# Kernel optimization log

Measured on AMD Instinct MI355X. Metric: run time of the kernel, lower is better.

Reference implementation:

```python
import jax, jax.numpy as jnp
import numpy as np

B, L, HIDDEN = 64, 200, 256
HEADS = 8
MAX_WIDTH = 5
EPS = 1e-5  # F.layer_norm default eps


def _ln(x):
    # F.layer_norm with no learned affine
    m = jnp.mean(x, axis=-1, keepdims=True)
    v = jnp.mean((x - m) ** 2, axis=-1, keepdims=True)
    return (x - m) * jax.lax.rsqrt(v + EPS)


def _area_pool(x, max_width, mode):
    # x: [B, H, L, D] -> pooled spans of widths 1..max_width (valid windows),
    # concatenated along the memory axis: M = sum_w (L - w + 1)
    Lx = x.shape[2]
    outs = []
    for w in range(1, max_width + 1):
        # [w, B, H, L-w+1, D] stack of shifted slices (w <= 5, tiny loop)
        win = jnp.stack([x[:, :, i:Lx - w + 1 + i, :] for i in range(w)], axis=0)
        if mode == 'max':
            outs.append(win.max(axis=0))
        elif mode == 'mean':
            outs.append(win.mean(axis=0))
        else:  # 'sum'
            outs.append(win.sum(axis=0))
    return jnp.concatenate(outs, axis=2)


def _mha_area(q_in, k_in, v_in, Wq, bq, Wk, bk, Wv, bv, Wo, bo):
    # per-head size equals hidden_size (key_query_size_hidden = hidden_size)
    Bq, Lq, _ = q_in.shape
    Dh = Wq.shape[1] // HEADS

    def split(x):
        return x.reshape(x.shape[0], x.shape[1], HEADS, Dh).transpose(0, 2, 1, 3)

    q = split(q_in @ Wq + bq)  # [B, H, Lq, Dh]
    k = split(k_in @ Wk + bk)
    v = split(v_in @ Wv + bv)
    k_area = _area_pool(k, MAX_WIDTH, 'max')   # aggr='max' key pooling
    v_area = _area_pool(v, MAX_WIDTH, 'sum')   # values pooled by sum (t2t default)
    scale = jnp.asarray(1.0 / np.sqrt(Dh), q.dtype)
    logits = jnp.einsum('bhqd,bhmd->bhqm', q, k_area) * scale
    attn = jax.nn.softmax(logits, axis=-1)  # dropout inactive at eval
    out = jnp.einsum('bhqm,bhmd->bhqd', attn, v_area)
    out = out.transpose(0, 2, 1, 3).reshape(Bq, Lq, HEADS * Dh)
    return out @ Wo + bo


def setup_inputs() -> dict:
    key = jax.random.key(0)
    ks = jax.random.split(key, 16)
    stdv = 1.0 / np.sqrt(HIDDEN)
    u = lambda k, shp: jax.random.uniform(k, shp, jnp.float32, -stdv, stdv)
    HD = HEADS * HIDDEN  # 2048
    return {
        'A': jax.random.normal(ks[0], (B, L, L), jnp.float32),
        'hidden': jax.random.normal(ks[1], (B, L, HIDDEN), jnp.float32),
        'Wq': u(ks[2], (HIDDEN, HD)), 'bq': u(ks[3], (HD,)),
        'Wk': u(ks[4], (HIDDEN, HD)), 'bk': u(ks[5], (HD,)),
        'Wv': u(ks[6], (HIDDEN, HD)), 'bv': u(ks[7], (HD,)),
        'Wo': u(ks[8], (HD, HIDDEN)), 'bo': u(ks[9], (HIDDEN,)),
        'W1': u(ks[10], (HIDDEN, 4 * HIDDEN)), 'b1': u(ks[11], (4 * HIDDEN,)),
        'W2': u(ks[12], (4 * HIDDEN, HIDDEN)), 'b2': u(ks[13], (HIDDEN,)),
    }


def reference(A, hidden, Wq, bq, Wk, bk, Wv, bv, Wo, bo, W1, b1, W2, b2):
    # step = 1 -> single ATTNCell; A is unused by ATTNCell (matches source)
    attn1 = _mha_area(hidden, hidden, hidden, Wq, bq, Wk, bk, Wv, bv, Wo, bo)
    attn1 = _ln(attn1 + hidden)
    attn2 = _mha_area(attn1, hidden, hidden, Wq, bq, Wk, bk, Wv, bv, Wo, bo)
    attn2 = _ln(attn1 + attn2)  # F.dropout inactive (eval)
    x = jax.nn.relu(attn2 @ W1 + b1) @ W2 + b2
    return _ln(attn2 + x)
```

## Files before the change

kernel.cpp:

```cpp
#include <hip/hip_runtime.h>
#include <hip/hip_bf16.h>
#include <cstdint>
#include <cstddef>

#define BATCH 64
#define LSEQ 200
#define HID 256
#define NH 8
#define DH 256
#define HD (NH*DH)
#define MROWS (BATCH*LSEQ)
#define EPS 1e-5f
#define CSCALE 0.09014195f

typedef unsigned short ushort_t;
typedef __attribute__((ext_vector_type(8))) short bf16x8;
typedef __attribute__((ext_vector_type(8))) unsigned short u16x8;
typedef __attribute__((ext_vector_type(4))) float f32x4;

__device__ __forceinline__ float b2f(ushort_t u) {
    union { unsigned int i; float f; } c; c.i = ((unsigned int)u) << 16; return c.f;
}
__device__ __forceinline__ ushort_t f2b(float f) {
    __hip_bfloat16 h = __float2bfloat16(f);
    union { __hip_bfloat16 h; ushort_t u; } c; c.h = h; return c.u;
}
__device__ __forceinline__ float to_f32(float x) { return x; }
__device__ __forceinline__ float to_f32(ushort_t x) { return b2f(x); }
__device__ __forceinline__ void store_val(float* p, float v) { *p = v; }
__device__ __forceinline__ void store_val(ushort_t* p, float v) { *p = f2b(v); }

__device__ __forceinline__ u16x8 bmax8(u16x8 a, u16x8 b) {
    union U { u16x8 v; __hip_bfloat162 h[4]; };
    U ua, ub, r; ua.v = a; ub.v = b;
    #pragma unroll
    for (int i = 0; i < 4; ++i) r.h[i] = __hmax2(ua.h[i], ub.h[i]);
    return r.v;
}
__device__ __forceinline__ u16x8 badd8(u16x8 a, u16x8 b) {
    union U { u16x8 v; __hip_bfloat162 h[4]; };
    U ua, ub, r; ua.v = a; ub.v = b;
    #pragma unroll
    for (int i = 0; i < 4; ++i) r.h[i] = __hadd2(ua.h[i], ub.h[i]);
    return r.v;
}

__device__ __forceinline__ void gll16(const void* g, void* l) {
    __builtin_amdgcn_global_load_lds(
        (const __attribute__((address_space(1))) unsigned int*)g,
        (__attribute__((address_space(3))) unsigned int*)l, 16, 0, 0);
}

template<bool RELU, int OMODE, bool SCALEC>
__global__ __launch_bounds__(256) void gemm_bt(
    const ushort_t* __restrict__ A, const ushort_t* __restrict__ Bt,
    const float* __restrict__ bias, ushort_t* __restrict__ C,
    int M, int N, int K)
{
    __shared__ ushort_t As[128 * 32];
    __shared__ ushort_t Bs[128 * 32];
    const int t = threadIdx.x;
    const int m0 = blockIdx.y * 128, n0 = blockIdx.x * 128;
    const int wave = t >> 6, lane = t & 63;
    const int l15 = lane & 15, lq = lane >> 4;
    const int wr = wave >> 1, wc = wave & 1;

    f32x4 acc[4][4];
    #pragma unroll
    for (int i = 0; i < 4; ++i)
        #pragma unroll
        for (int j = 0; j < 4; ++j) acc[i][j] = (f32x4){0.f, 0.f, 0.f, 0.f};

    for (int k0 = 0; k0 < K; k0 += 32) {
        __syncthreads();
        #pragma unroll
        for (int i = 0; i < 2; ++i) {
            int li = i * 256 + t;
            int ml = li >> 2, cp = li & 3;
            int cg = cp ^ ((ml ^ (ml >> 2)) & 3);
            gll16(A + (size_t)(m0 + ml) * K + k0 + cg * 8, &As[li * 8]);
        }
        #pragma unroll
        for (int i = 0; i < 2; ++i) {
            int li = i * 256 + t;
            int nl = li >> 2, cp = li & 3;
            int cg = cp ^ ((nl ^ (nl >> 2)) & 3);
            gll16(Bt + (size_t)(n0 + nl) * K + k0 + cg * 8, &Bs[li * 8]);
        }
        __syncthreads();
        bf16x8 af[4], bfr[4];
        #pragma unroll
        for (int i = 0; i < 4; ++i) {
            int r = wr * 64 + i * 16 + l15;
            int pc = lq ^ ((r ^ (r >> 2)) & 3);
            af[i] = *(const bf16x8*)&As[r * 32 + pc * 8];
        }
// ... 2 lines not shown
            int r = wc * 64 + j * 16 + l15;
            int pc = lq ^ ((r ^ (r >> 2)) & 3);
            bfr[j] = *(const bf16x8*)&Bs[r * 32 + pc * 8];
        }
        #pragma unroll
        for (int i = 0; i < 4; ++i)
            #pragma unroll
            for (int j = 0; j < 4; ++j)
                acc[i][j] = __builtin_amdgcn_mfma_f32_16x16x32_bf16(af[i], bfr[j], acc[i][j], 0, 0, 0);
    }
    if (OMODE == 2) {
        #pragma unroll
        for (int i = 0; i < 4; ++i) {
            int mbase = m0 + wr * 64 + i * 16 + 4 * lq;
            int bb = (int)(((unsigned)mbase * 5243u) >> 20);
            int ll = mbase - bb * 200;
            #pragma unroll
            for (int j = 0; j < 4; ++j) {
                int n = n0 + wc * 64 + j * 16 + l15;
                float bsv = bias[n];
                ushort4 o4;
                o4.x = f2b(acc[i][j][0] + bsv); o4.y = f2b(acc[i][j][1] + bsv);
                o4.z = f2b(acc[i][j][2] + bsv); o4.w = f2b(acc[i][j][3] + bsv);
                size_t addr = ((size_t)(bb * NH + (n >> 8)) * 256 + (n & 255)) * LSEQ + ll;
                *(ushort4*)&C[addr] = o4;
            }
        }
    } else {
        #pragma unroll
        for (int i = 0; i < 4; ++i) {
            #pragma unroll
            for (int e = 0; e < 4; ++e) {
                int m = m0 + wr * 64 + i * 16 + 4 * lq + e;
                #pragma unroll
                for (int j = 0; j < 4; ++j) {
                    int n = n0 + wc * 64 + j * 16 + l15;
                    float v = acc[i][j][e] + bias[n];
                    if (RELU) v = fmaxf(v, 0.f);
                    if (SCALEC) v *= CSCALE;
                    if (OMODE == 1) {
                        int bb = (int)(((unsigned)m * 5243u) >> 20);
                        int ll = m - bb * 200;
                        size_t addr = ((((size_t)(bb * NH + (n >> 8))) * LSEQ + ll) << 8) + (n & 255);
                        C[addr] = f2b(v);
                    } else {
                        C[(size_t)m * N + n] = f2b(v);
                    }
                }
            }
        }
    }
}

__global__ __launch_bounds__(512, 2) void attn_mfma16(
    const ushort_t* __restrict__ Q, const ushort_t* __restrict__ Khm,
    const ushort_t* __restrict__ Vt, ushort_t* __restrict__ O)
{
    const int id = blockIdx.x;
    const int xcd = id & 7, slot_ = id >> 3;
    const int qt = slot_ & 1;
    const int bh = ((slot_ >> 1) << 3) + xcd;
    const int b = bh >> 3, h = bh & 7;
    const int q0 = qt * 128;
    const int t = threadIdx.x;
    const int wave = t >> 6, lane = t & 63;
    const int l15 = lane & 15, lq = lane >> 4;

    __shared__ ushort_t Ks[64 * 256];
    __shared__ ushort_t Vs[256 * 64];

    const ushort_t* kbh = Khm + (size_t)bh * LSEQ * DH;
    const ushort_t* vtb = Vt + (size_t)bh * DH * LSEQ;
    const ushort_t* qbh = Q + ((size_t)b * LSEQ) * HD + h * DH;
    const int qrow = q0 + wave * 16 + l15;

    bf16x8 qf[8];
    if (qrow < LSEQ) {
        const ushort_t* qp = qbh + (size_t)qrow * HD + 8 * lq;
        #pragma unroll
        for (int g = 0; g < 8; ++g) qf[g] = *(const bf16x8*)(qp + 32 * g);
    } else {
        bf16x8 zf = {0,0,0,0,0,0,0,0};
        #pragma unroll
        for (int g = 0; g < 8; ++g) qf[g] = zf;
    }

    f32x4 oacc[16];
    #pragma unroll
    for (int i = 0; i < 16; ++i) oacc[i] = (f32x4){0.f, 0.f, 0.f, 0.f};
    float l_part = 0.f;
    float carry[4];
    #pragma unroll
    for (int e = 0; e < 4; ++e) carry[e] = 0.f;

    const int dc = t & 31, mb = t >> 5;
    const int vd = t >> 1, vh = t & 1;

    auto shift1 = [&](float T[4][4]) {
        float up0 = __shfl(T[0][3], (lane - 16) & 63);
        float up1 = __shfl(T[1][3], (lane - 16) & 63);
        float up2 = __shfl(T[2][3], (lane - 16) & 63);
        float up3 = __shfl(T[3][3], (lane - 16) & 63);
        #pragma unroll
        for (int ms = 0; ms < 4; ++ms) {
            T[ms][3] = T[ms][2]; T[ms][2] = T[ms][1]; T[ms][1] = T[ms][0];
        }
        T[3][0] = (lq > 0) ? up3 : up2;
        T[2][0] = (lq > 0) ? up2 : up1;
        T[1][0] = (lq > 0) ? up1 : up0;
        T[0][0] = (lq > 0) ? up0 : 0.f;
    };

    auto pv32 = [&](const float P[4][4]) {
        unsigned int w[8];
        #pragma unroll
        for (int ms = 0; ms < 4; ++ms) {
            asm("v_cvt_pk_bf16_f32 %0, %1, %2" : "=v"(w[2*ms])   : "v"(P[ms][0]), "v"(P[ms][1]));
            asm("v_cvt_pk_bf16_f32 %0, %1, %2" : "=v"(w[2*ms+1]) : "v"(P[ms][2]), "v"(P[ms][3]));
        }
        union FR { unsigned int u[4]; bf16x8 v; };
        FR f0, f1;
        f0.u[0] = w[0]; f0.u[1] = w[1]; f0.u[2] = w[2]; f0.u[3] = w[3];
        f1.u[0] = w[4]; f1.u[1] = w[5]; f1.u[2] = w[6]; f1.u[3] = w[7];
        const bf16x8 pf0 = f0.v, pf1 = f1.v;
        __builtin_amdgcn_s_setprio(1);
        #pragma unroll
        for (int dt = 0; dt < 16; ++dt) {
            const int d = dt * 16 + l15;
            const int p0 = lq ^ (d & 7);
            const int p1 = (lq + 4) ^ (d & 7);
            oacc[dt] = __builtin_amdgcn_mfma_f32_16x16x32_bf16(
                           pf0, *(const bf16x8*)&Vs[d * 64 + p0 * 8], oacc[dt], 0, 0, 0);
            oacc[dt] = __builtin_amdgcn_mfma_f32_16x16x32_bf16(
                           pf1, *(const bf16x8*)&Vs[d * 64 + p1 * 8], oacc[dt], 0, 0, 0);
        }
        __builtin_amdgcn_s_setprio(0);
    };

    for (int ti = 0; ti < 3; ++ti) {
        const int st0 = ti * 64;
        float Pagg[4][4];
        {
            float pin0 = __shfl(carry[0], (lane + 48) & 63);
            float pin1 = __shfl(carry[1], (lane + 48) & 63);
            float pin2 = __shfl(carry[2], (lane + 48) & 63);
            float pin3 = __shfl(carry[3], (lane + 48) & 63);
            #pragma unroll
            for (int ms = 0; ms < 4; ++ms)
                #pragma unroll
                for (int e = 0; e < 4; ++e) Pagg[ms][e] = 0.f;
            if (lq == 0) {
                Pagg[0][0] = pin0; Pagg[0][1] = pin1; Pagg[0][2] = pin2; Pagg[0][3] = pin3;
            }
            #pragma unroll
            for (int e = 0; e < 4; ++e) carry[e] = 0.f;
        }
        #pragma unroll
        for (int cls = 0; cls < 5; ++cls) {
            u16x8 kf[4];
            #pragma unroll
            for (int k4 = 0; k4 < 4; ++k4)
                kf[k4] = *(const u16x8*)(kbh + (size_t)(st0 + mb + 16 * k4 + cls) * DH + dc * 8);
            u16x8 vc[4];
            if (cls == 0) {
                const ushort_t* vrow = vtb + (size_t)vd * LSEQ + st0 + vh * 32;
                #pragma unroll
                for (int c2 = 0; c2 < 4; ++c2) vc[c2] = *(const u16x8*)(vrow + c2 * 8);
            }
            __syncthreads();

            #pragma unroll
            for (int k4 = 0; k4 < 4; ++k4) {
                int m = mb + 16 * k4;
                ushort_t* kp = &Ks[m * 256 + ((dc ^ (m & 15)) * 8)];
                *(u16x8*)kp = (cls == 0) ? kf[k4] : bmax8(*(const u16x8*)kp, kf[k4]);
            }
            if (cls == 0) {
                #pragma unroll
                for (int cl = 0; cl < 4; ++cl) {
                    const int cg = vh * 4 + cl;
                    const int kc = (cg >> 2) * 4 + (cg & 1) * 2;
                    const int par4 = ((cg >> 1) & 1) * 4;
                    union VH { u16x8 v; ushort4 hh[2]; } nv;
                    nv.v = vc[cl];
                    *(ushort4*)&Vs[vd * 64 + ((kc ^ (vd & 7)) * 8) + par4] = nv.hh[0];
                    *(ushort4*)&Vs[vd * 64 + (((kc + 1) ^ (vd & 7)) * 8) + par4] = nv.hh[1];
                }
            }
            __syncthreads();

            f32x4 sacc[4];
            __builtin_amdgcn_s_setprio(1);
            #pragma unroll
            for (int ms = 0; ms < 4; ++ms) {
                f32x4 s = (f32x4){0.f, 0.f, 0.f, 0.f};
                const int row = ms * 16 + l15;
                #pragma unroll
                for (int g = 0; g < 8; ++g) {
                    const int phys = (lq + 4 * g) ^ l15;
                    s = __builtin_amdgcn_mfma_f32_16x16x32_bf16(
                            *(const bf16x8*)&Ks[row * 256 + phys * 8], qf[g], s, 0, 0, 0);
                }
                sacc[ms] = s;
            }
            __builtin_amdgcn_s_setprio(0);

            float Pc[4][4];
            #pragma unroll
            for (int ms = 0; ms < 4; ++ms)
                #pragma unroll
                for (int e = 0; e < 4; ++e) {
                    float pe = __builtin_exp2f(sacc[ms][e]);
                    l_part += pe;
                    Pc[ms][e] = pe;
                    Pagg[ms][e] += pe;
                }
            if (cls >= 1) {
                float T[4][4];
                #pragma unroll
                for (int ms = 0; ms < 4; ++ms)
                    #pragma unroll
                    for (int e = 0; e < 4; ++e) T[ms][e] = Pc[ms][e];
                #pragma unroll
                for (int u = 1; u <= 4; ++u) {
                    if (u <= cls) {
                        shift1(T);
                        #pragma unroll
                        for (int ms = 0; ms < 4; ++ms)
                            #pragma unroll
                            for (int e = 0; e < 4; ++e) Pagg[ms][e] += T[ms][e];
                    }
                }
            }
            #pragma unroll
            for (int i = 0; i < 4; ++i)
                #pragma unroll
                for (int e = 0; e < 4; ++e)
                    if (cls >= 4 + i - e) carry[i] += Pc[3][e];

            if (cls == 4) pv32(Pagg);
        }
    }

    {
        __syncthreads();
        if (mb < 8) {
            u16x8 krun = *(const u16x8*)(kbh + (size_t)(192 + mb) * DH + dc * 8);
            const u16x8 kz = {0,0,0,0,0,0,0,0};
            #pragma unroll
            for (int k8 = 0; k8 < 8; ++k8) {
                const bool v = (k8 <= 4) && (mb <= 7 - k8);
                if (k8 > 0 && v)
                    krun = bmax8(krun, *(const u16x8*)(kbh + (size_t)(192 + mb + k8) * DH + dc * 8));
                int slot = k8 * 8 + mb;
                *(u16x8*)&Ks[slot * 256 + ((dc ^ (slot & 15)) * 8)] = v ? krun : kz;
            }
        }
        {
            u16x8 v0 = *(const u16x8*)(vtb + (size_t)vd * LSEQ + 192);
            float f[8];
            #pragma unroll
            for (int e = 0; e < 8; ++e) f[e] = b2f(v0[e]);
            #pragma unroll
            for (int cl = 0; cl < 4; ++cl) {
                const int c = vh * 4 + cl;
                union VH { u16x8 v; ushort4 hh[2]; } ov;
                #pragma unroll
                for (int j = 0; j < 8; ++j) ov.v[j] = 0;
                if (c <= 4) {
                    #pragma unroll
                    for (int j = 0; j < 8; ++j) {
                        if (j <= 7 - c) {
                            float acc = 0.f;
                            #pragma unroll
                            for (int u = 0; u <= 4; ++u)
                                if (u <= c) acc += f[j + u];
                            ov.v[j] = f2b(acc);
                        }
                    }
                } else if (c == 5) {
                    #pragma unroll
                    for (int j = 0; j < 4; ++j) ov.v[j] = v0[j];
                }
                const int kc = (c >> 2) * 4 + (c & 1) * 2;
                const int par4 = ((c >> 1) & 1) * 4;
                *(ushort4*)&Vs[vd * 64 + ((kc ^ (vd & 7)) * 8) + par4] = ov.hh[0];
                *(ushort4*)&Vs[vd * 64 + (((kc + 1) ^ (vd & 7)) * 8) + par4] = ov.hh[1];
            }
        }
        __syncthreads();

        f32x4 sacc[4];
        __builtin_amdgcn_s_setprio(1);
        #pragma unroll
        for (int ms = 0; ms < 4; ++ms) {
            f32x4 s = (f32x4){0.f, 0.f, 0.f, 0.f};
            const int row = ms * 16 + l15;
            #pragma unroll
            for (int g = 0; g < 8; ++g) {
                const int phys = (lq + 4 * g) ^ l15;
                s = __builtin_amdgcn_mfma_f32_16x16x32_bf16(
                        *(const bf16x8*)&Ks[row * 256 + phys * 8], qf[g], s, 0, 0, 0);
            }
            sacc[ms] = s;
        }
        __builtin_amdgcn_s_setprio(0);

        float pullc[4];
        #pragma unroll
        for (int e = 0; e < 4; ++e) pullc[e] = __shfl(carry[e], (lane + 16) & 63);
        float Pt[4][4];
        #pragma unroll
        for (int ms = 0; ms < 4; ++ms)
            #pragma unroll
            for (int e = 0; e < 4; ++e) {
                const int slot = ms * 16 + 4 * lq + e;
                const bool inval = ((slot & 7) > 7 - (slot >> 3)) || ((slot >> 3) > 4);
                float pe = __builtin_exp2f(inval ? -1e30f : sacc[ms][e]);
                l_part += pe;
                float pfrag = pe;
                if (ms == 2 && lq == 2) pfrag = pullc[e];
                Pt[ms][e] = pfrag;
            }
        pv32(Pt);
    }

    l_part += __shfl_xor(l_part, 16);
    l_part += __shfl_xor(l_part, 32);
    const float inv = 1.f / l_part;

    ushort_t* ob = O + ((size_t)b * LSEQ) * HD + h * DH;
    #pragma unroll
    for (int e = 0; e < 4; ++e) {
        const int q = q0 + wave * 16 + 4 * lq + e;
        const float linv = __shfl(inv, 4 * lq + e);
        if (q < LSEQ) {
            #pragma unroll
            for (int dt = 0; dt < 16; ++dt)
                ob[(size_t)q * HD + dt * 16 + l15] = f2b(oacc[dt][e] * linv);
        }
    }
}

template<typename TR, typename TO>
__global__ __launch_bounds__(256) void residual_ln(
    const ushort_t* __restrict__ X, const TR* __restrict__ R, TO* __restrict__ Out)
{
    const int row = blockIdx.x;
    const int t = threadIdx.x;
    const size_t base = (size_t)row * HID;
    float v = b2f(X[base + t]) + to_f32(R[base + t]);
    float s = v, q = v * v;
    #pragma unroll
    for (int o = 32; o > 0; o >>= 1) {
        s += __shfl_xor(s, o, 64);
        q += __shfl_xor(q, o, 64);
    }
    __shared__ float ss[4], sq[4];
    const int wave = t >> 6, lane = t & 63;
    if (lane == 0) { ss[wave] = s; sq[wave] = q; }
    __syncthreads();
    s = ss[0] + ss[1] + ss[2] + ss[3];
    q = sq[0] + sq[1] + sq[2] + sq[3];
    float mean = s * (1.f / HID);
    float var  = q * (1.f / HID) - mean * mean;
    store_val(&Out[base + t], (v - mean) * rsqrtf(var + EPS));
}

__global__ __launch_bounds__(256) void cvt_f32_bf16(const float* __restrict__ in,
                                                    ushort_t* __restrict__ out) {
    const int i = (blockIdx.x * 256 + threadIdx.x) * 4;
    float4 v = *(const float4*)(in + i);
    ushort4 o;
    o.x = f2b(v.x); o.y = f2b(v.y); o.z = f2b(v.z); o.w = f2b(v.w);
    *(ushort4*)(out + i) = o;
}

__global__ __launch_bounds__(256) void wtrans(const float* __restrict__ W,
                                              ushort_t* __restrict__ Wt, int K, int N) {
// ... 11 lines not shown
}

extern "C" void kernel_launch(void* const* d_in, const int* in_sizes, int n_in,
                              void* d_out, int out_size, void* d_ws, size_t ws_size,
                              hipStream_t stream) {
    const float* hidden = (const float*)d_in[1];
    const float* Wq = (const float*)d_in[2];  const float* bq = (const float*)d_in[3];
    const float* Wk = (const float*)d_in[4];  const float* bk = (const float*)d_in[5];
    const float* Wv = (const float*)d_in[6];  const float* bv = (const float*)d_in[7];
    const float* Wo = (const float*)d_in[8];  const float* bo = (const float*)d_in[9];
    const float* W1 = (const float*)d_in[10]; const float* b1 = (const float*)d_in[11];
    const float* W2 = (const float*)d_in[12]; const float* b2 = (const float*)d_in[13];
    float* out = (float*)d_out;

    constexpr size_t SZ_BF   = (size_t)MROWS * HD * 2;
    constexpr size_t SZ_HBF  = (size_t)MROWS * HID * 2;
    constexpr size_t SZ_WQKV = (size_t)HID * HD * 2;
    constexpr size_t SZ_W12  = (size_t)HID * 4 * HID * 2;
    char* ws = (char*)d_ws;
    size_t off = 0;
    ushort_t* kb   = (ushort_t*)(ws + off); off += SZ_BF;
    ushort_t* vt   = (ushort_t*)(ws + off); off += SZ_BF;
    ushort_t* qo   = (ushort_t*)(ws + off); off += SZ_BF;
    ushort_t* hb   = (ushort_t*)(ws + off); off += SZ_HBF;
    ushort_t* at1  = (ushort_t*)(ws + off); off += SZ_HBF;
    ushort_t* at2  = (ushort_t*)(ws + off); off += SZ_HBF;
    ushort_t* proj = (ushort_t*)(ws + off); off += SZ_HBF;
    ushort_t* WtQ  = (ushort_t*)(ws + off); off += SZ_WQKV;
    ushort_t* WtK  = (ushort_t*)(ws + off); off += SZ_WQKV;
    ushort_t* WtV  = (ushort_t*)(ws + off); off += SZ_WQKV;
    ushort_t* WtO  = (ushort_t*)(ws + off); off += SZ_WQKV;
    ushort_t* Wt1  = (ushort_t*)(ws + off); off += SZ_W12;
    ushort_t* Wt2  = (ushort_t*)(ws + off); off += SZ_W12;
    if (ws_size < off) return;
    ushort_t* ffn1 = qo;

    dim3 blk(256);
    cvt_f32_bf16<<<MROWS * HID / 1024, blk, 0, stream>>>(hidden, hb);
    wtrans<<<dim3(HD / 32, HID / 32), blk, 0, stream>>>(Wq, WtQ, HID, HD);
    wtrans<<<dim3(HD / 32, HID / 32), blk, 0, stream>>>(Wk, WtK, HID, HD);
    wtrans<<<dim3(HD / 32, HID / 32), blk, 0, stream>>>(Wv, WtV, HID, HD);
    wtrans<<<dim3(HID / 32, HD / 32), blk, 0, stream>>>(Wo, WtO, HD, HID);
    wtrans<<<dim3(4 * HID / 32, HID / 32), blk, 0, stream>>>(W1, Wt1, HID, 4 * HID);
    wtrans<<<dim3(HID / 32, 4 * HID / 32), blk, 0, stream>>>(W2, Wt2, 4 * HID, HID);

    const dim3 gProj(HD / 128, MROWS / 128);
    const dim3 gOut(HID / 128, MROWS / 128);
    const dim3 gF1(4 * HID / 128, MROWS / 128);

    gemm_bt<false, 1, false><<<gProj, blk, 0, stream>>>(hb, WtK, bk, kb, MROWS, HD, HID);
    gemm_bt<false, 2, false><<<gProj, blk, 0, stream>>>(hb, WtV, bv, vt, MROWS, HD, HID);

    gemm_bt<false, 0, true><<<gProj, blk, 0, stream>>>(hb, WtQ, bq, qo, MROWS, HD, HID);
    attn_mfma16<<<2 * BATCH * NH, 512, 0, stream>>>(qo, kb, vt, qo);
    gemm_bt<false, 0, false><<<gOut, blk, 0, stream>>>(qo, WtO, bo, proj, MROWS, HID, HD);
    residual_ln<float, ushort_t><<<MROWS, blk, 0, stream>>>(proj, hidden, at1);

    gemm_bt<false, 0, true><<<gProj, blk, 0, stream>>>(at1, WtQ, bq, qo, MROWS, HD, HID);
    attn_mfma16<<<2 * BATCH * NH, 512, 0, stream>>>(qo, kb, vt, qo);
    gemm_bt<false, 0, false><<<gOut, blk, 0, stream>>>(qo, WtO, bo, proj, MROWS, HID, HD);
    residual_ln<ushort_t, ushort_t><<<MROWS, blk, 0, stream>>>(proj, at1, at2);

    gemm_bt<true, 0, false><<<gF1, blk, 0, stream>>>(at2, Wt1, b1, ffn1, MROWS, 4 * HID, HID);
    gemm_bt<false, 0, false><<<gOut, blk, 0, stream>>>(ffn1, Wt2, b2, proj, MROWS, HID, 4 * HID);
    residual_ln<ushort_t, float><<<MROWS, blk, 0, stream>>>(proj, at2, out);
}
```

Baseline: 902.3 us.

## Double-buffer K/V shared tiles in area attention to overlap loads with MFMA

Result: slower. 1.153 ms (+27.8%).

```diff
diff --git a/kernel.cpp b/kernel.cpp
--- a/kernel.cpp
+++ b/kernel.cpp
@@ -150,7 +150,7 @@
     }
 }
 
-__global__ __launch_bounds__(512, 2) void attn_mfma16(
+__global__ __launch_bounds__(512, 2) void attn_mfma17(
     const ushort_t* __restrict__ Q, const ushort_t* __restrict__ Khm,
     const ushort_t* __restrict__ Vt, ushort_t* __restrict__ O)
 {
@@ -164,8 +164,8 @@
     const int wave = t >> 6, lane = t & 63;
     const int l15 = lane & 15, lq = lane >> 4;
 
-    __shared__ ushort_t Ks[64 * 256];
-    __shared__ ushort_t Vs[256 * 64];
+    __shared__ ushort_t Ks[2 * 64 * 256];
+    __shared__ ushort_t Vs[2 * 256 * 64];
 
     const ushort_t* kbh = Khm + (size_t)bh * LSEQ * DH;
     const ushort_t* vtb = Vt + (size_t)bh * DH * LSEQ;
@@ -186,13 +186,47 @@
     f32x4 oacc[16];
     #pragma unroll
     for (int i = 0; i < 16; ++i) oacc[i] = (f32x4){0.f, 0.f, 0.f, 0.f};
-    float l_part = 0.f;
+    float l4[4];
+    #pragma unroll
+    for (int e = 0; e < 4; ++e) l4[e] = 0.f;
     float carry[4];
     #pragma unroll
     for (int e = 0; e < 4; ++e) carry[e] = 0.f;
 
     const int dc = t & 31, mb = t >> 5;
     const int vd = t >> 1, vh = t & 1;
+
+    u16x8 kr[4];
+
+    auto loadK = [&](u16x8* kf, int row0) {
+        #pragma unroll
+        for (int k4 = 0; k4 < 4; ++k4)
+            kf[k4] = *(const u16x8*)(kbh + (size_t)(row0 + mb + 16 * k4) * DH + dc * 8);
+    };
+    auto storeK = [&](int bo, const u16x8* kf) {
+        #pragma unroll
+        for (int k4 = 0; k4 < 4; ++k4) {
+            int m = mb + 16 * k4;
+            *(u16x8*)&Ks[bo + m * 256 + ((dc ^ (m & 15)) * 8)] = kf[k4];
+        }
+    };
+    auto loadV = [&](u16x8* vc, int s0) {
+        const ushort_t* vrow = vtb + (size_t)vd * LSEQ + s0 + vh * 32;
+        #pragma unroll
+        for (int c2 = 0; c2 < 4; ++c2) vc[c2] = *(const u16x8*)(vrow + c2 * 8);
+    };
+    auto storeV = [&](int bo, const u16x8* vc) {
+        #pragma unroll
+        for (int cl = 0; cl < 4; ++cl) {
+            const int cg = vh * 4 + cl;
+            const int kc = (cg >> 2) * 4 + (cg & 1) * 2;
+            const int par4 = ((cg >> 1) & 1) * 4;
+            union VH { u16x8 v; ushort4 hh[2]; } nv;
+            nv.v = vc[cl];
+            *(ushort4*)&Vs[bo + vd * 64 + ((kc ^ (vd & 7)) * 8) + par4] = nv.hh[0];
+            *(ushort4*)&Vs[bo + vd * 64 + (((kc + 1) ^ (vd & 7)) * 8) + par4] = nv.hh[1];
+        }
+    };
 
     auto shift1 = [&](float T[4][4]) {
         float up0 = __shfl(T[0][3], (lane - 16) & 63);
@@ -209,7 +243,7 @@
         T[0][0] = (lq > 0) ? up0 : 0.f;
     };
 
-    auto pv32 = [&](const float P[4][4]) {
+    auto pv32 = [&](int bo, const float P[4][4]) {
         unsigned int w[8];
         #pragma unroll
         for (int ms = 0; ms < 4; ++ms) {
@@ -228,15 +262,29 @@
             const int p0 = lq ^ (d & 7);
             const int p1 = (lq + 4) ^ (d & 7);
             oacc[dt] = __builtin_amdgcn_mfma_f32_16x16x32_bf16(
-                           pf0, *(const bf16x8*)&Vs[d * 64 + p0 * 8], oacc[dt], 0, 0, 0);
+                           pf0, *(const bf16x8*)&Vs[bo + d * 64 + p0 * 8], oacc[dt], 0, 0, 0);
             oacc[dt] = __builtin_amdgcn_mfma_f32_16x16x32_bf16(
-                           pf1, *(const bf16x8*)&Vs[d * 64 + p1 * 8], oacc[dt], 0, 0, 0);
+                           pf1, *(const bf16x8*)&Vs[bo + d * 64 + p1 * 8], oacc[dt], 0, 0, 0);
         }
         __builtin_amdgcn_s_setprio(0);
     };
 
+    {
+        u16x8 kf[4];
+        u16x8 vc[4];
+        loadK(kf, 0);
+        loadV(vc, 0);
+        #pragma unroll
+        for (int k4 = 0; k4 < 4; ++k4) kr[k4] = kf[k4];
+        storeK(0, kr);
+        storeV(0, vc);
+    }
+    __syncthreads();
+
+    int cb = 0;
     for (int ti = 0; ti < 3; ++ti) {
         const int st0 = ti * 64;
+        const int vbo = (ti & 1) * 16384;
         float Pagg[4][4];
         {
             float pin0 = __shfl(carry[0], (lane + 48) & 63);
@@ -255,38 +303,16 @@
         }
         #pragma unroll
         for (int cls = 0; cls < 5; ++cls) {
+            const int kbo = cb * 16384;
+            const bool lastS = (cls == 4) && (ti == 2);
             u16x8 kf[4];
-            #pragma unroll
-            for (int k4 = 0; k4 < 4; ++k4)
-                kf[k4] = *(const u16x8*)(kbh + (size_t)(st0 + mb + 16 * k4 + cls) * DH + dc * 8);
             u16x8 vc[4];
-            if (cls == 0) {
-                const ushort_t* vrow = vtb + (size_t)vd * LSEQ + st0 + vh * 32;
-                #pragma unroll
-                for (int c2 = 0; c2 < 4; ++c2) vc[c2] = *(const u16x8*)(vrow + c2 * 8);
-            }
-            __syncthreads();
-
-            #pragma unroll
-            for (int k4 = 0; k4 < 4; ++k4) {
-                int m = mb + 16 * k4;
-                ushort_t* kp = &Ks[m * 256 + ((dc ^ (m & 15)) * 8)];
-                *(u16x8*)kp = (cls == 0) ? kf[k4] : bmax8(*(const u16x8*)kp, kf[k4]);
-            }
-            if (cls == 0) {
-                #pragma unroll
-                for (int cl = 0; cl < 4; ++cl) {
-                    const int cg = vh * 4 + cl;
-                    const int kc = (cg >> 2) * 4 + (cg & 1) * 2;
-                    const int par4 = ((cg >> 1) & 1) * 4;
-                    union VH { u16x8 v; ushort4 hh[2]; } nv;
-                    nv.v = vc[cl];
-                    *(ushort4*)&Vs[vd * 64 + ((kc ^ (vd & 7)) * 8) + par4] = nv.hh[0];
-                    *(ushort4*)&Vs[vd * 64 + (((kc + 1) ^ (vd & 7)) * 8) + par4] = nv.hh[1];
-                }
-            }
-            __syncthreads();
-
+            if (cls < 4) {
+                loadK(kf, st0 + cls + 1);
+            } else if (!lastS) {
+                loadK(kf, st0 + 64);
+                loadV(vc, st0 + 64);
+            }
             f32x4 sacc[4];
             __builtin_amdgcn_s_setprio(1);
             #pragma unroll
@@ -297,7 +323,7 @@
                 for (int g = 0; g < 8; ++g) {
                     const int phys = (lq + 4 * g) ^ l15;
                     s = __builtin_amdgcn_mfma_f32_16x16x32_bf16(
-                            *(const bf16x8*)&Ks[row * 256 + phys * 8], qf[g], s, 0, 0, 0);
+                            *(const bf16x8*)&Ks[kbo + row * 256 + phys * 8], qf[g], s, 0, 0, 0);
                 }
                 sacc[ms] = s;
             }
@@ -309,7 +335,7 @@
                 #pragma unroll
                 for (int e = 0; e < 4; ++e) {
                     float pe = __builtin_exp2f(sacc[ms][e]);
-                    l_part += pe;
+                    l4[e] += pe;
                     Pc[ms][e] = pe;
                     Pagg[ms][e] += pe;
                 }
@@ -336,22 +362,34 @@
                 for (int e = 0; e < 4; ++e)
                     if (cls >= 4 + i - e) carry[i] += Pc[3][e];
 
-            if (cls == 4) pv32(Pagg);
+            if (cls == 4) pv32(vbo, Pagg);
+
+            if (cls < 4) {
+                #pragma unroll
+                for (int k4 = 0; k4 < 4; ++k4) kr[k4] = bmax8(kr[k4], kf[k4]);
+                storeK(kbo ^ 16384, kr);
+            } else if (!lastS) {
+                #pragma unroll
+                for (int k4 = 0; k4 < 4; ++k4) kr[k4] = kf[k4];
+                storeK(kbo ^ 16384, kr);
+                storeV(vbo ^ 16384, vc);
+            }
+            __syncthreads();
+            cb ^= 1;
         }
     }
 
     {
-        __syncthreads();
         if (mb < 8) {
             u16x8 krun = *(const u16x8*)(kbh + (size_t)(192 + mb) * DH + dc * 8);
             const u16x8 kz = {0,0,0,0,0,0,0,0};
             #pragma unroll
             for (int k8 = 0; k8 < 8; ++k8) {
-                const bool v = (k8 <= 4) && (mb <= 7 - k8);
-                if (k8 > 0 && v)
+                const bool vv = (k8 <= 4) && (mb <= 7 - k8);
+                if (k8 > 0 && vv)
                     krun = bmax8(krun, *(const u16x8*)(kbh + (size_t)(192 + mb + k8) * DH + dc * 8));
                 int slot = k8 * 8 + mb;
-                *(u16x8*)&Ks[slot * 256 + ((dc ^ (slot & 15)) * 8)] = v ? krun : kz;
+                *(u16x8*)&Ks[16384 + slot * 256 + ((dc ^ (slot & 15)) * 8)] = vv ? krun : kz;
             }
         }
         {
@@ -382,8 +420,8 @@
                 }
                 const int kc = (c >> 2) * 4 + (c & 1) * 2;
                 const int par4 = ((c >> 1) & 1) * 4;
-                *(ushort4*)&Vs[vd * 64 + ((kc ^ (vd & 7)) * 8) + par4] = ov.hh[0];
-                *(ushort4*)&Vs[vd * 64 + (((kc + 1) ^ (vd & 7)) * 8) + par4] = ov.hh[1];
+                *(ushort4*)&Vs[16384 + vd * 64 + ((kc ^ (vd & 7)) * 8) + par4] = ov.hh[0];
+                *(ushort4*)&Vs[16384 + vd * 64 + (((kc + 1) ^ (vd & 7)) * 8) + par4] = ov.hh[1];
             }
         }
         __syncthreads();
@@ -398,7 +436,7 @@
             for (int g = 0; g < 8; ++g) {
                 const int phys = (lq + 4 * g) ^ l15;
                 s = __builtin_amdgcn_mfma_f32_16x16x32_bf16(
-                        *(const bf16x8*)&Ks[row * 256 + phys * 8], qf[g], s, 0, 0, 0);
+                        *(const bf16x8*)&Ks[16384 + row * 256 + phys * 8], qf[g], s, 0, 0, 0);
             }
             sacc[ms] = s;
         }
@@ -415,14 +453,15 @@
                 const int slot = ms * 16 + 4 * lq + e;
                 const bool inval = ((slot & 7) > 7 - (slot >> 3)) || ((slot >> 3) > 4);
                 float pe = __builtin_exp2f(inval ? -1e30f : sacc[ms][e]);
-                l_part += pe;
+                l4[e] += pe;
                 float pfrag = pe;
                 if (ms == 2 && lq == 2) pfrag = pullc[e];
                 Pt[ms][e] = pfrag;
             }
-        pv32(Pt);
-    }
-
+        pv32(16384, Pt);
+    }
+
+    float l_part = (l4[0] + l4[1]) + (l4[2] + l4[3]);
     l_part += __shfl_xor(l_part, 16);
     l_part += __shfl_xor(l_part, 32);
     const float inv = 1.f / l_part;
@@ -540,12 +579,12 @@
     gemm_bt<false, 2, false><<<gProj, blk, 0, stream>>>(hb, WtV, bv, vt, MROWS, HD, HID);
 
     gemm_bt<false, 0, true><<<gProj, blk, 0, stream>>>(hb, WtQ, bq, qo, MROWS, HD, HID);
-    attn_mfma16<<<2 * BATCH * NH, 512, 0, stream>>>(qo, kb, vt, qo);
+    attn_mfma17<<<2 * BATCH * NH, 512, 0, stream>>>(qo, kb, vt, qo);
     gemm_bt<false, 0, false><<<gOut, blk, 0, stream>>>(qo, WtO, bo, proj, MROWS, HID, HD);
     residual_ln<float, ushort_t><<<MROWS, blk, 0, stream>>>(proj, hidden, at1);
 
     gemm_bt<false, 0, true><<<gProj, blk, 0, stream>>>(at1, WtQ, bq, qo, MROWS, HD, HID);
-    attn_mfma16<<<2 * BATCH * NH, 512, 0, stream>>>(qo, kb, vt, qo);
+    attn_mfma17<<<2 * BATCH * NH, 512, 0, stream>>>(qo, kb, vt, qo);
     gemm_bt<false, 0, false><<<gOut, blk, 0, stream>>>(qo, WtO, bo, proj, MROWS, HID, HD);
     residual_ln<ushort_t, ushort_t><<<MROWS, blk, 0, stream>>>(proj, at1, at2);
 
```

## Split attention into 64-row query tiles with 256-thread blocks

Applied to the files above, without the earlier changes.

New measurement: 1.100 ms. 1.22x slower.

```diff
diff --git a/kernel.cpp b/kernel.cpp
--- a/kernel.cpp
+++ b/kernel.cpp
@@ -150,16 +150,16 @@
     }
 }
 
-__global__ __launch_bounds__(512, 2) void attn_mfma16(
+__global__ __launch_bounds__(256, 2) void attn_mfma19(
     const ushort_t* __restrict__ Q, const ushort_t* __restrict__ Khm,
     const ushort_t* __restrict__ Vt, ushort_t* __restrict__ O)
 {
     const int id = blockIdx.x;
     const int xcd = id & 7, slot_ = id >> 3;
-    const int qt = slot_ & 1;
-    const int bh = ((slot_ >> 1) << 3) + xcd;
+    const int qt = slot_ & 3;
+    const int bh = ((slot_ >> 2) << 3) + xcd;
     const int b = bh >> 3, h = bh & 7;
-    const int q0 = qt * 128;
+    const int q0 = qt * 64;
     const int t = threadIdx.x;
     const int wave = t >> 6, lane = t & 63;
     const int l15 = lane & 15, lq = lane >> 4;
@@ -192,7 +192,7 @@
     for (int e = 0; e < 4; ++e) carry[e] = 0.f;
 
     const int dc = t & 31, mb = t >> 5;
-    const int vd = t >> 1, vh = t & 1;
+    const int vd = t;
 
     auto shift1 = [&](float T[4][4]) {
         float up0 = __shfl(T[0][3], (lane - 16) & 63);
@@ -235,6 +235,15 @@
         __builtin_amdgcn_s_setprio(0);
     };
 
+    auto storeVchunk = [&](int cg, u16x8 val) {
+        const int kc = (cg >> 2) * 4 + (cg & 1) * 2;
+        const int par4 = ((cg >> 1) & 1) * 4;
+        union VH { u16x8 v; ushort4 hh[2]; } nv;
+        nv.v = val;
+        *(ushort4*)&Vs[vd * 64 + ((kc ^ (vd & 7)) * 8) + par4] = nv.hh[0];
+        *(ushort4*)&Vs[vd * 64 + (((kc + 1) ^ (vd & 7)) * 8) + par4] = nv.hh[1];
+    };
+
     for (int ti = 0; ti < 3; ++ti) {
         const int st0 = ti * 64;
         float Pagg[4][4];
@@ -257,33 +266,36 @@
         for (int cls = 0; cls < 5; ++cls) {
             u16x8 kf[4];
             #pragma unroll
-            for (int k4 = 0; k4 < 4; ++k4)
-                kf[k4] = *(const u16x8*)(kbh + (size_t)(st0 + mb + 16 * k4 + cls) * DH + dc * 8);
+            for (int k8 = 0; k8 < 4; ++k8)
+                kf[k8] = *(const u16x8*)(kbh + (size_t)(st0 + mb + 8 * k8 + cls) * DH + dc * 8);
             u16x8 vc[4];
             if (cls == 0) {
-                const ushort_t* vrow = vtb + (size_t)vd * LSEQ + st0 + vh * 32;
+                const ushort_t* vrow = vtb + (size_t)vd * LSEQ + st0;
                 #pragma unroll
                 for (int c2 = 0; c2 < 4; ++c2) vc[c2] = *(const u16x8*)(vrow + c2 * 8);
             }
             __syncthreads();
 
             #pragma unroll
-            for (int k4 = 0; k4 < 4; ++k4) {
-                int m = mb + 16 * k4;
+            for (int k8 = 0; k8 < 4; ++k8) {
+                int m = mb + 8 * k8;
                 ushort_t* kp = &Ks[m * 256 + ((dc ^ (m & 15)) * 8)];
-                *(u16x8*)kp = (cls == 0) ? kf[k4] : bmax8(*(const u16x8*)kp, kf[k4]);
+                *(u16x8*)kp = (cls == 0) ? kf[k8] : bmax8(*(const u16x8*)kp, kf[k8]);
+            }
+            #pragma unroll
+            for (int k8 = 4; k8 < 8; ++k8) {
+                u16x8 kv = *(const u16x8*)(kbh + (size_t)(st0 + mb + 8 * k8 + cls) * DH + dc * 8);
+                int m = mb + 8 * k8;
+                ushort_t* kp = &Ks[m * 256 + ((dc ^ (m & 15)) * 8)];
+                *(u16x8*)kp = (cls == 0) ? kv : bmax8(*(const u16x8*)kp, kv);
             }
             if (cls == 0) {
                 #pragma unroll
-                for (int cl = 0; cl < 4; ++cl) {
-                    const int cg = vh * 4 + cl;
-                    const int kc = (cg >> 2) * 4 + (cg & 1) * 2;
-                    const int par4 = ((cg >> 1) & 1) * 4;
-                    union VH { u16x8 v; ushort4 hh[2]; } nv;
-                    nv.v = vc[cl];
-                    *(ushort4*)&Vs[vd * 64 + ((kc ^ (vd & 7)) * 8) + par4] = nv.hh[0];
-                    *(ushort4*)&Vs[vd * 64 + (((kc + 1) ^ (vd & 7)) * 8) + par4] = nv.hh[1];
-                }
+                for (int cg = 0; cg < 4; ++cg) storeVchunk(cg, vc[cg]);
+                const ushort_t* vrow = vtb + (size_t)vd * LSEQ + st0;
+                #pragma unroll
+                for (int cg = 4; cg < 8; ++cg)
+                    storeVchunk(cg, *(const u16x8*)(vrow + cg * 8));
             }
             __syncthreads();
 
@@ -342,16 +354,16 @@
 
     {
         __syncthreads();
-        if (mb < 8) {
+        {
             u16x8 krun = *(const u16x8*)(kbh + (size_t)(192 + mb) * DH + dc * 8);
             const u16x8 kz = {0,0,0,0,0,0,0,0};
             #pragma unroll
             for (int k8 = 0; k8 < 8; ++k8) {
-                const bool v = (k8 <= 4) && (mb <= 7 - k8);
-                if (k8 > 0 && v)
+                const bool vv = (k8 <= 4) && (mb <= 7 - k8);
+                if (k8 > 0 && vv)
                     krun = bmax8(krun, *(const u16x8*)(kbh + (size_t)(192 + mb + k8) * DH + dc * 8));
                 int slot = k8 * 8 + mb;
-                *(u16x8*)&Ks[slot * 256 + ((dc ^ (slot & 15)) * 8)] = v ? krun : kz;
+                *(u16x8*)&Ks[slot * 256 + ((dc ^ (slot & 15)) * 8)] = vv ? krun : kz;
             }
         }
         {
@@ -360,11 +372,10 @@
             #pragma unroll
             for (int e = 0; e < 8; ++e) f[e] = b2f(v0[e]);
             #pragma unroll
-            for (int cl = 0; cl < 4; ++cl) {
-                const int c = vh * 4 + cl;
-                union VH { u16x8 v; ushort4 hh[2]; } ov;
-                #pragma unroll
-                for (int j = 0; j < 8; ++j) ov.v[j] = 0;
+            for (int c = 0; c < 8; ++c) {
+                u16x8 ov;
+                #pragma unroll
+                for (int j = 0; j < 8; ++j) ov[j] = 0;
                 if (c <= 4) {
                     #pragma unroll
                     for (int j = 0; j < 8; ++j) {
@@ -373,17 +384,14 @@
                             #pragma unroll
                             for (int u = 0; u <= 4; ++u)
                                 if (u <= c) acc += f[j + u];
-                            ov.v[j] = f2b(acc);
+                            ov[j] = f2b(acc);
                         }
                     }
                 } else if (c == 5) {
                     #pragma unroll
-                    for (int j = 0; j < 4; ++j) ov.v[j] = v0[j];
+                    for (int j = 0; j < 4; ++j) ov[j] = v0[j];
                 }
-                const int kc = (c >> 2) * 4 + (c & 1) * 2;
-                const int par4 = ((c >> 1) & 1) * 4;
-                *(ushort4*)&Vs[vd * 64 + ((kc ^ (vd & 7)) * 8) + par4] = ov.hh[0];
-                *(ushort4*)&Vs[vd * 64 + (((kc + 1) ^ (vd & 7)) * 8) + par4] = ov.hh[1];
+                storeVchunk(c, ov);
             }
         }
         __syncthreads();
@@ -540,12 +548,12 @@
     gemm_bt<false, 2, false><<<gProj, blk, 0, stream>>>(hb, WtV, bv, vt, MROWS, HD, HID);
 
     gemm_bt<false, 0, true><<<gProj, blk, 0, stream>>>(hb, WtQ, bq, qo, MROWS, HD, HID);
-    attn_mfma16<<<2 * BATCH * NH, 512, 0, stream>>>(qo, kb, vt, qo);
+    attn_mfma19<<<4 * BATCH * NH, 256, 0, stream>>>(qo, kb, vt, qo);
     gemm_bt<false, 0, false><<<gOut, blk, 0, stream>>>(qo, WtO, bo, proj, MROWS, HID, HD);
     residual_ln<float, ushort_t><<<MROWS, blk, 0, stream>>>(proj, hidden, at1);
 
     gemm_bt<false, 0, true><<<gProj, blk, 0, stream>>>(at1, WtQ, bq, qo, MROWS, HD, HID);
-    attn_mfma16<<<2 * BATCH * NH, 512, 0, stream>>>(qo, kb, vt, qo);
+    attn_mfma19<<<4 * BATCH * NH, 256, 0, stream>>>(qo, kb, vt, qo);
     gemm_bt<false, 0, false><<<gOut, blk, 0, stream>>>(qo, WtO, bo, proj, MROWS, HID, HD);
     residual_ln<ushort_t, ushort_t><<<MROWS, blk, 0, stream>>>(proj, at1, at2);
 
```

## Double-buffer pooled key classes in LDS and process two width classes per sync

Applied to the files above, without the earlier changes.

After: 972.9 us. 7.8% more time.

```diff
diff --git a/kernel.cpp b/kernel.cpp
--- a/kernel.cpp
+++ b/kernel.cpp
@@ -35,13 +35,6 @@
     U ua, ub, r; ua.v = a; ub.v = b;
     #pragma unroll
     for (int i = 0; i < 4; ++i) r.h[i] = __hmax2(ua.h[i], ub.h[i]);
-    return r.v;
-}
-__device__ __forceinline__ u16x8 badd8(u16x8 a, u16x8 b) {
-    union U { u16x8 v; __hip_bfloat162 h[4]; };
-    U ua, ub, r; ua.v = a; ub.v = b;
-    #pragma unroll
-    for (int i = 0; i < 4; ++i) r.h[i] = __hadd2(ua.h[i], ub.h[i]);
     return r.v;
 }
 
@@ -150,7 +143,7 @@
     }
 }
 
-__global__ __launch_bounds__(512, 2) void attn_mfma16(
+__global__ __launch_bounds__(512, 2) void attn_mfma20(
     const ushort_t* __restrict__ Q, const ushort_t* __restrict__ Khm,
     const ushort_t* __restrict__ Vt, ushort_t* __restrict__ O)
 {
@@ -164,7 +157,7 @@
     const int wave = t >> 6, lane = t & 63;
     const int l15 = lane & 15, lq = lane >> 4;
 
-    __shared__ ushort_t Ks[64 * 256];
+    __shared__ ushort_t Ks[2 * 64 * 256];
     __shared__ ushort_t Vs[256 * 64];
 
     const ushort_t* kbh = Khm + (size_t)bh * LSEQ * DH;
@@ -186,27 +179,79 @@
     f32x4 oacc[16];
     #pragma unroll
     for (int i = 0; i < 16; ++i) oacc[i] = (f32x4){0.f, 0.f, 0.f, 0.f};
-    float l_part = 0.f;
+    float l4[4];
+    #pragma unroll
+    for (int e = 0; e < 4; ++e) l4[e] = 0.f;
     float carry[4];
     #pragma unroll
     for (int e = 0; e < 4; ++e) carry[e] = 0.f;
+    float Pagg[4][4];
 
     const int dc = t & 31, mb = t >> 5;
     const int vd = t >> 1, vh = t & 1;
-
-    auto shift1 = [&](float T[4][4]) {
-        float up0 = __shfl(T[0][3], (lane - 16) & 63);
-        float up1 = __shfl(T[1][3], (lane - 16) & 63);
-        float up2 = __shfl(T[2][3], (lane - 16) & 63);
-        float up3 = __shfl(T[3][3], (lane - 16) & 63);
+    const int srow = ((mb >> 2) << 4) + (mb & 3);
+
+    auto kOff = [&](int k4) {
+        int m = mb + 16 * k4;
+        return m * 256 + ((dc ^ (m & 15)) * 8);
+    };
+
+    auto qk = [&](int bo, f32x4* sacc) {
+        __builtin_amdgcn_s_setprio(1);
         #pragma unroll
         for (int ms = 0; ms < 4; ++ms) {
-            T[ms][3] = T[ms][2]; T[ms][2] = T[ms][1]; T[ms][1] = T[ms][0];
-        }
-        T[3][0] = (lq > 0) ? up3 : up2;
-        T[2][0] = (lq > 0) ? up2 : up1;
-        T[1][0] = (lq > 0) ? up1 : up0;
-        T[0][0] = (lq > 0) ? up0 : 0.f;
+            f32x4 s = (f32x4){0.f, 0.f, 0.f, 0.f};
+            const int row = ms * 16 + l15;
+            #pragma unroll
+            for (int g = 0; g < 8; ++g) {
+                const int phys = (lq + 4 * g) ^ l15;
+                s = __builtin_amdgcn_mfma_f32_16x16x32_bf16(
+                        *(const bf16x8*)&Ks[bo + row * 256 + phys * 8], qf[g], s, 0, 0, 0);
+            }
+            sacc[ms] = s;
+        }
+        __builtin_amdgcn_s_setprio(0);
+    };
+
+    auto smClass = [&](const f32x4* sacc, int cls) {
+        float Pc[4][4];
+        #pragma unroll
+        for (int ms = 0; ms < 4; ++ms)
+            #pragma unroll
+            for (int e = 0; e < 4; ++e) {
+                float pe = __builtin_exp2f(sacc[ms][e]);
+                l4[e] += pe;
+                Pc[ms][e] = pe;
+                Pagg[ms][e] += pe;
+            }
+        if (cls >= 1) {
+            float T[4][4];
+            #pragma unroll
+            for (int ms = 0; ms < 4; ++ms)
+                #pragma unroll
+                for (int e = 0; e < 4; ++e) T[ms][e] = Pc[ms][e];
+            #pragma unroll
+            for (int u = 1; u <= 4; ++u) {
+                if (u <= cls) {
+                    float up = __shfl(T[3][3], (lane - 16) & 63);
+                    #pragma unroll
+                    for (int ms = 3; ms >= 0; --ms) {
+                        float nv = (ms > 0) ? T[ms - 1][3] : ((lq > 0) ? up : 0.f);
+                        T[ms][3] = T[ms][2]; T[ms][2] = T[ms][1]; T[ms][1] = T[ms][0];
+                        T[ms][0] = nv;
+                    }
+                    #pragma unroll
+                    for (int ms = 0; ms < 4; ++ms)
+                        #pragma unroll
+                        for (int e = 0; e < 4; ++e) Pagg[ms][e] += T[ms][e];
+                }
+            }
+        }
+        #pragma unroll
+        for (int i = 0; i < 4; ++i)
+            #pragma unroll
+            for (int e = 0; e < 4; ++e)
+                if (cls >= 4 + i - e) carry[i] += Pc[3][e];
     };
 
     auto pv32 = [&](const float P[4][4]) {
@@ -235,9 +280,37 @@
         __builtin_amdgcn_s_setprio(0);
     };
 
+    auto storeVchunk = [&](int kc, u16x8 val) {
+        *(u16x8*)&Vs[vd * 64 + ((kc ^ (vd & 7)) * 8)] = val;
+    };
+
+    {
+        u16x8 r0[4], r1[4], vc[4];
+        #pragma unroll
+        for (int k4 = 0; k4 < 4; ++k4) {
+            const int s = srow + 4 * k4;
+            r0[k4] = *(const u16x8*)(kbh + (size_t)(s) * DH + dc * 8);
+            r1[k4] = *(const u16x8*)(kbh + (size_t)(s + 1) * DH + dc * 8);
+        }
+        const ushort_t* vrow = vtb + (size_t)vd * LSEQ + vh * 32;
+        #pragma unroll
+        for (int cl = 0; cl < 4; ++cl) vc[cl] = *(const u16x8*)(vrow + cl * 8);
+        #pragma unroll
+        for (int k4 = 0; k4 < 4; ++k4) {
+            const int off = kOff(k4);
+            *(u16x8*)&Ks[off] = r0[k4];
+            *(u16x8*)&Ks[16384 + off] = bmax8(r0[k4], r1[k4]);
+        }
+        #pragma unroll
+        for (int cl = 0; cl < 4; ++cl) {
+            const int cg = vh * 4 + cl;
+            storeVchunk((cg & 1) * 4 + (cg >> 1), vc[cl]);
+        }
+    }
+    __syncthreads();
+
     for (int ti = 0; ti < 3; ++ti) {
         const int st0 = ti * 64;
-        float Pagg[4][4];
         {
             float pin0 = __shfl(carry[0], (lane + 48) & 63);
             float pin1 = __shfl(carry[1], (lane + 48) & 63);
@@ -253,157 +326,130 @@
             #pragma unroll
             for (int e = 0; e < 4; ++e) carry[e] = 0.f;
         }
-        #pragma unroll
-        for (int cls = 0; cls < 5; ++cls) {
-            u16x8 kf[4];
-            #pragma unroll
-            for (int k4 = 0; k4 < 4; ++k4)
-                kf[k4] = *(const u16x8*)(kbh + (size_t)(st0 + mb + 16 * k4 + cls) * DH + dc * 8);
-            u16x8 vc[4];
-            if (cls == 0) {
-                const ushort_t* vrow = vtb + (size_t)vd * LSEQ + st0 + vh * 32;
+        {
+            f32x4 sa[4], sb[4];
+            qk(0, sa); qk(16384, sb);
+            smClass(sa, 0); smClass(sb, 1);
+        }
+        {
+            u16x8 r2[4], r3[4];
+            #pragma unroll
+            for (int k4 = 0; k4 < 4; ++k4) {
+                const int s = st0 + srow + 4 * k4;
+                r2[k4] = *(const u16x8*)(kbh + (size_t)(s + 2) * DH + dc * 8);
+                r3[k4] = *(const u16x8*)(kbh + (size_t)(s + 3) * DH + dc * 8);
+            }
+            __syncthreads();
+            #pragma unroll
+            for (int k4 = 0; k4 < 4; ++k4) {
+                const int off = kOff(k4);
+                u16x8 c2 = bmax8(*(const u16x8*)&Ks[16384 + off], r2[k4]);
+                *(u16x8*)&Ks[off] = c2;
+                *(u16x8*)&Ks[16384 + off] = bmax8(c2, r3[k4]);
+            }
+            __syncthreads();
+        }
+        {
+            f32x4 sa[4], sb[4];
+            qk(0, sa); qk(16384, sb);
+            smClass(sa, 2); smClass(sb, 3);
+        }
+        {
+            u16x8 r4[4];
+            #pragma unroll
+            for (int k4 = 0; k4 < 4; ++k4) {
+                const int s = st0 + srow + 4 * k4;
+                r4[k4] = *(const u16x8*)(kbh + (size_t)(s + 4) * DH + dc * 8);
+            }
+            __syncthreads();
+            #pragma unroll
+            for (int k4 = 0; k4 < 4; ++k4) {
+                const int off = kOff(k4);
+                *(u16x8*)&Ks[off] = bmax8(*(const u16x8*)&Ks[16384 + off], r4[k4]);
+            }
+            __syncthreads();
+        }
+        {
+            f32x4 sa[4];
+            qk(0, sa);
+            smClass(sa, 4);
+            pv32(Pagg);
+        }
+        if (ti < 2) {
+            const int nt0 = st0 + 64;
+            u16x8 r0[4], r1[4], vc[4];
+            #pragma unroll
+            for (int k4 = 0; k4 < 4; ++k4) {
+                const int s = nt0 + srow + 4 * k4;
+                r0[k4] = *(const u16x8*)(kbh + (size_t)(s) * DH + dc * 8);
+                r1[k4] = *(const u16x8*)(kbh + (size_t)(s + 1) * DH + dc * 8);
+            }
+            const ushort_t* vrow = vtb + (size_t)vd * LSEQ + nt0 + vh * 32;
+            #pragma unroll
+            for (int cl = 0; cl < 4; ++cl) vc[cl] = *(const u16x8*)(vrow + cl * 8);
+            __syncthreads();
+            #pragma unroll
+            for (int k4 = 0; k4 < 4; ++k4) {
+                const int off = kOff(k4);
+                *(u16x8*)&Ks[off] = r0[k4];
+                *(u16x8*)&Ks[16384 + off] = bmax8(r0[k4], r1[k4]);
+            }
+            #pragma unroll
+            for (int cl = 0; cl < 4; ++cl) {
+                const int cg = vh * 4 + cl;
+                storeVchunk((cg & 1) * 4 + (cg >> 1), vc[cl]);
+            }
+            __syncthreads();
+        } else {
+            u16x8 v0 = *(const u16x8*)(vtb + (size_t)vd * LSEQ + 192);
+            __syncthreads();
+            if (mb < 8) {
+                u16x8 krun = *(const u16x8*)(kbh + (size_t)(192 + mb) * DH + dc * 8);
+                const u16x8 kz = {0,0,0,0,0,0,0,0};
                 #pragma unroll
-                for (int c2 = 0; c2 < 4; ++c2) vc[c2] = *(const u16x8*)(vrow + c2 * 8);
-            }
-            __syncthreads();
-
-            #pragma unroll
-            for (int k4 = 0; k4 < 4; ++k4) {
-                int m = mb + 16 * k4;
-                ushort_t* kp = &Ks[m * 256 + ((dc ^ (m & 15)) * 8)];
-                *(u16x8*)kp = (cls == 0) ? kf[k4] : bmax8(*(const u16x8*)kp, kf[k4]);
-            }
-            if (cls == 0) {
+                for (int k8 = 0; k8 < 8; ++k8) {
+                    const bool vv = (k8 <= 4) && (mb <= 7 - k8);
+                    if (k8 > 0 && vv)
+                        krun = bmax8(krun, *(const u16x8*)(kbh + (size_t)(192 + mb + k8) * DH + dc * 8));
+                    int slot = k8 * 8 + mb;
+                    *(u16x8*)&Ks[slot * 256 + ((dc ^ (slot & 15)) * 8)] = vv ? krun : kz;
+                }
+            }
+            {
+                float f[8];
                 #pragma unroll
-                for (int cl = 0; cl < 4; ++cl) {
-                    const int cg = vh * 4 + cl;
-                    const int kc = (cg >> 2) * 4 + (cg & 1) * 2;
-                    const int par4 = ((cg >> 1) & 1) * 4;
-                    union VH { u16x8 v; ushort4 hh[2]; } nv;
-                    nv.v = vc[cl];
-                    *(ushort4*)&Vs[vd * 64 + ((kc ^ (vd & 7)) * 8) + par4] = nv.hh[0];
-                    *(ushort4*)&Vs[vd * 64 + (((kc + 1) ^ (vd & 7)) * 8) + par4] = nv.hh[1];
-                }
-            }
-            __syncthreads();
-
-            f32x4 sacc[4];
-            __builtin_amdgcn_s_setprio(1);
-            #pragma unroll
-            for (int ms = 0; ms < 4; ++ms) {
-                f32x4 s = (f32x4){0.f, 0.f, 0.f, 0.f};
-                const int row = ms * 16 + l15;
+                for (int e = 0; e < 8; ++e) f[e] = b2f(v0[e]);
                 #pragma unroll
-                for (int g = 0; g < 8; ++g) {
-                    const int phys = (lq + 4 * g) ^ l15;
-                    s = __builtin_amdgcn_mfma_f32_16x16x32_bf16(
-                            *(const bf16x8*)&Ks[row * 256 + phys * 8], qf[g], s, 0, 0, 0);
-                }
-                sacc[ms] = s;
-            }
-            __builtin_amdgcn_s_setprio(0);
-
-            float Pc[4][4];
-            #pragma unroll
-            for (int ms = 0; ms < 4; ++ms)
-                #pragma unroll
-                for (int e = 0; e < 4; ++e) {
-                    float pe = __builtin_exp2f(sacc[ms][e]);
-                    l_part += pe;
-                    Pc[ms][e] = pe;
-                    Pagg[ms][e] += pe;
-                }
-            if (cls >= 1) {
-                float T[4][4];
-                #pragma unroll
-                for (int ms = 0; ms < 4; ++ms)
+                for (int ck = 0; ck < 4; ++ck) {
+                    const int kc = vh * 4 + ck;
+                    const int cls_lo = 4 * (kc >> 2) + ((kc >> 1) & 1);
+                    const int offb = 4 * (kc & 1);
+                    u16x8 ov;
                     #pragma unroll
-                    for (int e = 0; e < 4; ++e) T[ms][e] = Pc[ms][e];
-                #pragma unroll
-                for (int u = 1; u <= 4; ++u) {
-                    if (u <= cls) {
-                        shift1(T);
-                        #pragma unroll
-                        for (int ms = 0; ms < 4; ++ms)
-                            #pragma unroll
-                            for (int e = 0; e < 4; ++e) Pagg[ms][e] += T[ms][e];
-                    }
-                }
-            }
-            #pragma unroll
-            for (int i = 0; i < 4; ++i)
-                #pragma unroll
-                for (int e = 0; e < 4; ++e)
-                    if (cls >= 4 + i - e) carry[i] += Pc[3][e];
-
-            if (cls == 4) pv32(Pagg);
-        }
-    }
-
-    {
-        __syncthreads();
-        if (mb < 8) {
-            u16x8 krun = *(const u16x8*)(kbh + (size_t)(192 + mb) * DH + dc * 8);
-            const u16x8 kz = {0,0,0,0,0,0,0,0};
-            #pragma unroll
-            for (int k8 = 0; k8 < 8; ++k8) {
-                const bool v = (k8 <= 4) && (mb <= 7 - k8);
-                if (k8 > 0 && v)
-                    krun = bmax8(krun, *(const u16x8*)(kbh + (size_t)(192 + mb + k8) * DH + dc * 8));
-                int slot = k8 * 8 + mb;
-                *(u16x8*)&Ks[slot * 256 + ((dc ^ (slot & 15)) * 8)] = v ? krun : kz;
-            }
-        }
-        {
-            u16x8 v0 = *(const u16x8*)(vtb + (size_t)vd * LSEQ + 192);
-            float f[8];
-            #pragma unroll
-            for (int e = 0; e < 8; ++e) f[e] = b2f(v0[e]);
-            #pragma unroll
-            for (int cl = 0; cl < 4; ++cl) {
-                const int c = vh * 4 + cl;
-                union VH { u16x8 v; ushort4 hh[2]; } ov;
-                #pragma unroll
-                for (int j = 0; j < 8; ++j) ov.v[j] = 0;
-                if (c <= 4) {
-                    #pragma unroll
-                    for (int j = 0; j < 8; ++j) {
-                        if (j <= 7 - c) {
-                            float acc = 0.f;
+                    for (int o = 0; o < 8; ++o) {
+                        const int cls = cls_lo + 2 * (o >> 2);
+                        const int off = offb + (o & 3);
+                        ushort_t val = 0;
+                        if (cls <= 4 && off <= 7 - cls) {
+                            float a = 0.f;
                             #pragma unroll
                             for (int u = 0; u <= 4; ++u)
-                                if (u <= c) acc += f[j + u];
-                            ov.v[j] = f2b(acc);
+                                if (u <= cls) a += f[off + u];
+                            val = f2b(a);
                         }
+                        if (kc == 6 && o < 4) val = v0[o];
+                        ov[o] = val;
                     }
-                } else if (c == 5) {
-                    #pragma unroll
-                    for (int j = 0; j < 4; ++j) ov.v[j] = v0[j];
+                    storeVchunk(kc, ov);
                 }
-                const int kc = (c >> 2) * 4 + (c & 1) * 2;
-                const int par4 = ((c >> 1) & 1) * 4;
-                *(ushort4*)&Vs[vd * 64 + ((kc ^ (vd & 7)) * 8) + par4] = ov.hh[0];
-                *(ushort4*)&Vs[vd * 64 + (((kc + 1) ^ (vd & 7)) * 8) + par4] = ov.hh[1];
-            }
-        }
-        __syncthreads();
-
+            }
+            __syncthreads();
+        }
+    }
+
+    {
         f32x4 sacc[4];
-        __builtin_amdgcn_s_setprio(1);
-        #pragma unroll
-        for (int ms = 0; ms < 4; ++ms) {
-            f32x4 s = (f32x4){0.f, 0.f, 0.f, 0.f};
-            const int row = ms * 16 + l15;
-            #pragma unroll
-            for (int g = 0; g < 8; ++g) {
-                const int phys = (lq + 4 * g) ^ l15;
-                s = __builtin_amdgcn_mfma_f32_16x16x32_bf16(
-                        *(const bf16x8*)&Ks[row * 256 + phys * 8], qf[g], s, 0, 0, 0);
-            }
-            sacc[ms] = s;
-        }
-        __builtin_amdgcn_s_setprio(0);
-
+        qk(0, sacc);
         float pullc[4];
         #pragma unroll
         for (int e = 0; e < 4; ++e) pullc[e] = __shfl(carry[e], (lane + 16) & 63);
@@ -415,7 +461,7 @@
                 const int slot = ms * 16 + 4 * lq + e;
                 const bool inval = ((slot & 7) > 7 - (slot >> 3)) || ((slot >> 3) > 4);
                 float pe = __builtin_exp2f(inval ? -1e30f : sacc[ms][e]);
-                l_part += pe;
+                l4[e] += pe;
                 float pfrag = pe;
                 if (ms == 2 && lq == 2) pfrag = pullc[e];
                 Pt[ms][e] = pfrag;
@@ -423,6 +469,7 @@
         pv32(Pt);
     }
 
+    float l_part = (l4[0] + l4[1]) + (l4[2] + l4[3]);
     l_part += __shfl_xor(l_part, 16);
     l_part += __shfl_xor(l_part, 32);
     const float inv = 1.f / l_part;
@@ -540,12 +587,12 @@
     gemm_bt<false, 2, false><<<gProj, blk, 0, stream>>>(hb, WtV, bv, vt, MROWS, HD, HID);
 
     gemm_bt<false, 0, true><<<gProj, blk, 0, stream>>>(hb, WtQ, bq, qo, MROWS, HD, HID);
-    attn_mfma16<<<2 * BATCH * NH, 512, 0, stream>>>(qo, kb, vt, qo);
+    attn_mfma20<<<2 * BATCH * NH, 512, 0, stream>>>(qo, kb, vt, qo);
     gemm_bt<false, 0, false><<<gOut, blk, 0, stream>>>(qo, WtO, bo, proj, MROWS, HID, HD);
     residual_ln<float, ushort_t><<<MROWS, blk, 0, stream>>>(proj, hidden, at1);
 
     gemm_bt<false, 0, true><<<gProj, blk, 0, stream>>>(at1, WtQ, bq, qo, MROWS, HD, HID);
-    attn_mfma16<<<2 * BATCH * NH, 512, 0, stream>>>(qo, kb, vt, qo);
+    attn_mfma20<<<2 * BATCH * NH, 512, 0, stream>>>(qo, kb, vt, qo);
     gemm_bt<false, 0, false><<<gOut, blk, 0, stream>>>(qo, WtO, bo, proj, MROWS, HID, HD);
     residual_ln<ushort_t, ushort_t><<<MROWS, blk, 0, stream>>>(proj, at1, at2);
 
```
